# Optimization experiments

Hardware: AMD Instinct MI355X
Metric: run time of the kernel (lower is better)

Reference implementation:

```python
import jax, jax.numpy as jnp
import numpy as np

# Compressed weight shape [O, I] represents a dense [m=2*O, k=2*I] matrix:
#  - 1:2 structured row sparsity: `indices` [O] gives the nonzero dense row ids
#  - 2:4 structured col sparsity: `metadata` [O, I] gives, for each compressed
#    element, its position (0..3) within its group of 4 dense columns
O, I = 4096, 2048          # compressed weight dims (out_features, in_features)
M_DIM, K_DIM = 2 * O, 2 * I  # dense GEMM dims m, k
N_TOK = 4096               # n = input.shape[0]
K_ACT = 2048               # number of active activation rows (multiple of 64)
PAD_MULT = 64


def setup_inputs() -> dict:
    key = jax.random.key(0)
    k1, k2, k3, k4, k5 = jax.random.split(key, 5)
    inp = jax.random.normal(k1, (N_TOK, K_ACT), dtype=jnp.float32)
    # unique, sorted active-feature indices into the dense k dimension
    idx = jnp.sort(jax.random.permutation(k2, K_DIM)[:K_ACT]).astype(jnp.int32)
    # compressed N:M weight values (original uses torch.rand -> uniform [0,1))
    weight = jax.random.uniform(k3, (O, I), dtype=jnp.float32)
    # 1:2 row sparsity: which O of the m dense rows are nonzero
    indices = jnp.sort(jax.random.permutation(k4, M_DIM)[:O]).astype(jnp.int32)
    # 2:4 metadata: per group of 4 dense columns, 2 distinct sorted positions
    G = I // 2
    scores = jax.random.uniform(k5, (O, G, 4))
    metadata = jnp.sort(jnp.argsort(scores, axis=-1)[..., :2], axis=-1)
    metadata = metadata.reshape(O, I).astype(jnp.int32)
    return {"input": inp, "idx": idx, "weight": weight,
            "indices": indices, "metadata": metadata}


def _padding_idx(idx, mult):
    # pad index list to a multiple of `mult` (static shapes)
    pad = (-idx.shape[0]) % mult
    return jnp.pad(idx, (0, pad)), pad


def reference(input, idx, weight, indices, metadata):
    O_, I_ = weight.shape
    m, k, n = 2 * O_, 2 * I_, input.shape[0]
    # ---- decompress N:M weight to dense [m, k] ----
    group_base = (jnp.arange(I_) // 2) * 4                 # [I]
    dense_cols = group_base[None, :] + metadata            # [O, I] in [0, k)
    W = jnp.zeros((m, k), weight.dtype).at[indices[:, None], dense_cols].set(weight)
    # ---- decompress sparse activation to dense B [k, n] ----
    idx_p, pad = _padding_idx(idx, PAD_MULT)
    vals = jnp.pad(input, ((0, 0), (0, pad)))              # [n, K_act+pad]
    B = jnp.zeros((k, n), input.dtype).at[idx_p].add(vals.T)
    # ---- sparse-sparse GEMM (dense-equivalent reference) ----
    return W @ B                                           # [m, n]
```

## Files before the change

kernel.cpp:

```cpp
#include <hip/hip_runtime.h>
#include <hip/hip_bf16.h>
#include <stdint.h>

#define O_DIM   4096
#define I_DIM   2048
#define M_DENSE 8192
#define K_DENSE 4096
#define N_TOK   4096
#define K_ACT   2048

typedef __bf16 bf16x8 __attribute__((ext_vector_type(8)));
typedef float  f32x4  __attribute__((ext_vector_type(4)));

__device__ __forceinline__ unsigned f2bf(float f) {
    unsigned u = __builtin_bit_cast(unsigned, f);
    return (u + 0x7FFFu + ((u >> 16) & 1u)) >> 16;
}

__device__ __forceinline__ void load16(const unsigned short* g, unsigned short* l) {
    __builtin_amdgcn_global_load_lds(
        (__attribute__((address_space(1))) void*)(g),
        (__attribute__((address_space(3))) void*)(l),
        16, 0, 0);
}

__global__ void zero_inactive(const int* __restrict__ indices, float4* __restrict__ out4) {
    int b = blockIdx.x;
    int lo = (b == 0) ? -1 : indices[b - 1];
    int hi = (b == O_DIM) ? M_DENSE : indices[b];
    for (int row = lo + 1; row < hi; ++row) {
        float4* dst = out4 + (size_t)row * (N_TOK / 4);
        for (int c = threadIdx.x; c < N_TOK / 4; c += 256)
            dst[c] = float4{0.f, 0.f, 0.f, 0.f};
    }
}

__global__ __launch_bounds__(256) void prep(const float* __restrict__ weight,
                                            const int* __restrict__ metadata,
                                            const int* __restrict__ idx,
                                            const float* __restrict__ input,
                                            uint4* __restrict__ A2,
                                            uint4* __restrict__ Bbt) {
    if (blockIdx.x >= O_DIM) {
        int gid = (blockIdx.x - O_DIM) * 256 + threadIdx.x;
        const float4* in = (const float4*)input;
        float4 a = in[2 * gid], b = in[2 * gid + 1];
        uint4 u;
        u.x = f2bf(a.x) | (f2bf(a.y) << 16);
        u.y = f2bf(a.z) | (f2bf(a.w) << 16);
        u.z = f2bf(b.x) | (f2bf(b.y) << 16);
        u.w = f2bf(b.z) | (f2bf(b.w) << 16);
        Bbt[gid] = u;
        return;
    }
    __shared__ int   smeta[I_DIM];
    __shared__ float sw[I_DIM];
    int o = blockIdx.x;
    const int4*   mrow = (const int4*)(metadata + (size_t)o * I_DIM);
    const float4* wrow = (const float4*)(weight + (size_t)o * I_DIM);
#pragma unroll
    for (int it = 0; it < I_DIM / 4 / 256; ++it) {
        int i = it * 256 + threadIdx.x;
        *(int4*)(smeta + i * 4) = mrow[i];
        *(float4*)(sw + i * 4)  = wrow[i];
    }
    __syncthreads();
    int j0 = threadIdx.x * 8;
    int4 c0 = *(const int4*)(idx + j0);
    int4 c1 = *(const int4*)(idx + j0 + 4);
    int cs[8] = {c0.x, c0.y, c0.z, c0.w, c1.x, c1.y, c1.z, c1.w};
    unsigned r[8];
#pragma unroll
    for (int u = 0; u < 8; ++u) {
        int c = cs[u];
        int g2 = (c >> 2) * 2;
        int pos = c & 3;
        int m0v = smeta[g2], m1v = smeta[g2 + 1];
        float v = (m0v == pos) ? sw[g2] : ((m1v == pos) ? sw[g2 + 1] : 0.0f);
        r[u] = f2bf(v);
    }
    uint4 packed;
    packed.x = r[0] | (r[1] << 16);
    packed.y = r[2] | (r[3] << 16);
    packed.z = r[4] | (r[5] << 16);
    packed.w = r[6] | (r[7] << 16);
    A2[((size_t)o * K_ACT + j0) >> 3] = packed;
}

__global__ __launch_bounds__(256, 4) void gemm_scatter(
        const unsigned short* __restrict__ A,
        const unsigned short* __restrict__ Bt,
        const int* __restrict__ indices,
        float* __restrict__ out) {
    constexpr int N = N_TOK, K = K_ACT;
    constexpr int TM = 128, TN = 128, BK = 64;
    __shared__ alignas(16) unsigned short sA[TM * BK];
    __shared__ alignas(16) unsigned short sB[TN * BK];

    const int t    = threadIdx.x;
    const int wave = t >> 6;
    const int lane = t & 63;
    const int m0 = blockIdx.y * TM;
    const int n0 = blockIdx.x * TN;

    const int rbase = t >> 3;
    const int sseg  = (t & 7) ^ (rbase & 7);
    const unsigned short* gA = A  + (size_t)(m0 + rbase) * K + sseg * 8;
    const unsigned short* gB = Bt + (size_t)(n0 + rbase) * K + sseg * 8;
    unsigned short* lA = sA + wave * 512;
    unsigned short* lB = sB + wave * 512;

    const int wm   = (wave >> 1) * 64;
    const int wn   = (wave & 1) * 64;
    const int quad = lane >> 4;
    const int lr   = lane & 15;
    const int lr7  = lr & 7;
    const int k0 = (quad ^ lr7) * 8;
    const int k1 = k0 ^ 32;

    f32x4 acc[4][4] = {};

    for (int kk = 0; kk < K; kk += BK) {
        __syncthreads();
#pragma unroll
        for (int q = 0; q < 4; ++q) {
            load16(gA + (size_t)q * (32 * K) + kk, lA + q * 2048);
            load16(gB + (size_t)q * (32 * K) + kk, lB + q * 2048);
        }
        __syncthreads();

        bf16x8 af[4], bf[4];
#pragma unroll
        for (int mi = 0; mi < 4; ++mi)
            af[mi] = *(const bf16x8*)(sA + (wm + mi * 16 + lr) * BK + k0);
#pragma unroll
        for (int ni = 0; ni < 4; ++ni)
            bf[ni] = *(const bf16x8*)(sB + (wn + ni * 16 + lr) * BK + k0);
#pragma unroll
        for (int mi = 0; mi < 4; ++mi)
#pragma unroll
            for (int ni = 0; ni < 4; ++ni)
                acc[mi][ni] = __builtin_amdgcn_mfma_f32_16x16x32_bf16(
                    af[mi], bf[ni], acc[mi][ni], 0, 0, 0);
#pragma unroll
        for (int mi = 0; mi < 4; ++mi)
            af[mi] = *(const bf16x8*)(sA + (wm + mi * 16 + lr) * BK + k1);
#pragma unroll
        for (int ni = 0; ni < 4; ++ni)
            bf[ni] = *(const bf16x8*)(sB + (wn + ni * 16 + lr) * BK + k1);
#pragma unroll
        for (int mi = 0; mi < 4; ++mi)
#pragma unroll
            for (int ni = 0; ni < 4; ++ni)
                acc[mi][ni] = __builtin_amdgcn_mfma_f32_16x16x32_bf16(
                    af[mi], bf[ni], acc[mi][ni], 0, 0, 0);
    }

#pragma unroll
    for (int mi = 0; mi < 4; ++mi) {
#pragma unroll
        for (int r = 0; r < 4; ++r) {
            int gm = m0 + wm + mi * 16 + quad * 4 + r;
            int orow = indices[gm];
            float* op = out + (size_t)orow * N + n0 + wn + lr;
#pragma unroll
            for (int ni = 0; ni < 4; ++ni)
                op[ni * 16] = acc[mi][ni][r];
        }
    }
}

extern "C" void kernel_launch(void* const* d_in, const int* in_sizes, int n_in,
                              void* d_out, int out_size, void* d_ws, size_t ws_size,
                              hipStream_t stream) {
    const float* input    = (const float*)d_in[0];
    const int*   idx      = (const int*)d_in[1];
    const float* weight   = (const float*)d_in[2];
    const int*   indices  = (const int*)d_in[3];
    const int*   metadata = (const int*)d_in[4];
    float* out = (float*)d_out;

    unsigned short* A2  = (unsigned short*)d_ws;
    unsigned short* Bbt = (unsigned short*)((char*)d_ws + (size_t)(16 << 20));

    zero_inactive<<<O_DIM + 1, 256, 0, stream>>>(indices, (float4*)out);
    prep<<<O_DIM + (N_TOK * K_ACT / 8) / 256, 256, 0, stream>>>(
        weight, metadata, idx, input, (uint4*)A2, (uint4*)Bbt);

    dim3 grid(N_TOK / 128, O_DIM / 128);
    gemm_scatter<<<grid, 256, 0, stream>>>(A2, Bbt, indices, out);
}
```

Baseline: 282.5 us.

## Rewrite GEMM as 256x256 tile, 8-wave, 4-stage pipelined kernel; fuse zeroing into prep

```diff
diff --git a/kernel.cpp b/kernel.cpp
--- a/kernel.cpp
+++ b/kernel.cpp
@@ -24,25 +24,29 @@
         16, 0, 0);
 }
 
-__global__ void zero_inactive(const int* __restrict__ indices, float4* __restrict__ out4) {
-    int b = blockIdx.x;
-    int lo = (b == 0) ? -1 : indices[b - 1];
-    int hi = (b == O_DIM) ? M_DENSE : indices[b];
-    for (int row = lo + 1; row < hi; ++row) {
-        float4* dst = out4 + (size_t)row * (N_TOK / 4);
-        for (int c = threadIdx.x; c < N_TOK / 4; c += 256)
-            dst[c] = float4{0.f, 0.f, 0.f, 0.f};
-    }
-}
-
 __global__ __launch_bounds__(256) void prep(const float* __restrict__ weight,
                                             const int* __restrict__ metadata,
                                             const int* __restrict__ idx,
                                             const float* __restrict__ input,
+                                            const int* __restrict__ indices,
                                             uint4* __restrict__ A2,
-                                            uint4* __restrict__ Bbt) {
-    if (blockIdx.x >= O_DIM) {
-        int gid = (blockIdx.x - O_DIM) * 256 + threadIdx.x;
+                                            uint4* __restrict__ Bbt,
+                                            float4* __restrict__ out4) {
+    const int CAST_BLKS = (N_TOK * K_ACT / 8) / 256;
+    int bx = blockIdx.x;
+    if (bx >= O_DIM + CAST_BLKS) {
+        int b = bx - (O_DIM + CAST_BLKS);
+        int lo = (b == 0) ? -1 : indices[b - 1];
+        int hi = (b == O_DIM) ? M_DENSE : indices[b];
+        for (int row = lo + 1; row < hi; ++row) {
+            float4* dst = out4 + (size_t)row * (N_TOK / 4);
+            for (int c = threadIdx.x; c < N_TOK / 4; c += 256)
+                dst[c] = float4{0.f, 0.f, 0.f, 0.f};
+        }
+        return;
+    }
+    if (bx >= O_DIM) {
+        int gid = (bx - O_DIM) * 256 + threadIdx.x;
         const float4* in = (const float4*)input;
         float4 a = in[2 * gid], b = in[2 * gid + 1];
         uint4 u;
@@ -55,7 +59,7 @@
     }
     __shared__ int   smeta[I_DIM];
     __shared__ float sw[I_DIM];
-    int o = blockIdx.x;
+    int o = bx;
     const int4*   mrow = (const int4*)(metadata + (size_t)o * I_DIM);
     const float4* wrow = (const float4*)(weight + (size_t)o * I_DIM);
 #pragma unroll
@@ -87,81 +91,116 @@
     A2[((size_t)o * K_ACT + j0) >> 3] = packed;
 }
 
-__global__ __launch_bounds__(256, 4) void gemm_scatter(
+__global__ __launch_bounds__(512, 2) void gemm8(
         const unsigned short* __restrict__ A,
         const unsigned short* __restrict__ Bt,
         const int* __restrict__ indices,
         float* __restrict__ out) {
     constexpr int N = N_TOK, K = K_ACT;
-    constexpr int TM = 128, TN = 128, BK = 64;
-    __shared__ alignas(16) unsigned short sA[TM * BK];
-    __shared__ alignas(16) unsigned short sB[TN * BK];
-
-    const int t    = threadIdx.x;
-    const int wave = t >> 6;
-    const int lane = t & 63;
-    const int m0 = blockIdx.y * TM;
-    const int n0 = blockIdx.x * TN;
-
-    const int rbase = t >> 3;
-    const int sseg  = (t & 7) ^ (rbase & 7);
-    const unsigned short* gA = A  + (size_t)(m0 + rbase) * K + sseg * 8;
-    const unsigned short* gB = Bt + (size_t)(n0 + rbase) * K + sseg * 8;
-    unsigned short* lA = sA + wave * 512;
-    unsigned short* lB = sB + wave * 512;
-
-    const int wm   = (wave >> 1) * 64;
-    const int wn   = (wave & 1) * 64;
+    constexpr int NT = K / 32;
+    __shared__ alignas(16) unsigned short lds[65536];
+    __shared__ int sidx[256];
+
+    const int tid  = threadIdx.x;
+    const int wave = tid >> 6;
+    const int lane = tid & 63;
     const int quad = lane >> 4;
     const int lr   = lane & 15;
-    const int lr7  = lr & 7;
-    const int k0 = (quad ^ lr7) * 8;
-    const int k1 = k0 ^ 32;
-
-    f32x4 acc[4][4] = {};
-
-    for (int kk = 0; kk < K; kk += BK) {
-        __syncthreads();
-#pragma unroll
-        for (int q = 0; q < 4; ++q) {
-            load16(gA + (size_t)q * (32 * K) + kk, lA + q * 2048);
-            load16(gB + (size_t)q * (32 * K) + kk, lB + q * 2048);
+    const int wm   = (wave >> 2) * 128;
+    const int wn   = (wave & 3) * 64;
+
+    const int bid = blockIdx.x;
+    const int xcd = bid & 7;
+    const int j   = bid >> 3;
+    const int m0  = (j & 15) * 256;
+    const int n0  = (xcd * 2 + (j >> 4)) * 256;
+
+    const int sr_ = tid >> 3;
+    const int cb_ = ((tid & 7) << 4) ^ (((sr_ >> 2) & 1) << 5);
+    const int rh_ = (cb_ >> 6) & 1;
+    const int ke_ = (cb_ & 63) >> 1;
+    const unsigned short* gA0 = A  + (size_t)(m0 + sr_ +      rh_ * 128) * K + ke_;
+    const unsigned short* gA1 = A  + (size_t)(m0 + sr_ + 64 + rh_ * 128) * K + ke_;
+    const unsigned short* gB0 = Bt + (size_t)(n0 + sr_ +      rh_ * 128) * K + ke_;
+    const unsigned short* gB1 = Bt + (size_t)(n0 + sr_ + 64 + rh_ * 128) * K + ke_;
+    unsigned short* dA = lds + wave * 512;
+    unsigned short* dB = lds + 32768 + wave * 512;
+
+    const int laA = wm + lr, srA = laA & 127;
+    const int offA0 = srA * 128 + ((((laA >> 7) << 6) + (quad << 4)) ^ (((srA >> 2) & 1) << 5));
+    const int laB = wn + lr, srB = laB & 127;
+    const int offB0 = srB * 128 + ((((laB >> 7) << 6) + (quad << 4)) ^ (((srB >> 2) & 1) << 5));
+    const char* ldsB = (const char*)lds;
+
+    if (tid < 256) sidx[tid] = indices[m0 + tid];
+
+#pragma unroll
+    for (int pt = 0; pt < 3; ++pt) {
+        load16(gA0 + pt * 32, dA + pt * 8192);
+        load16(gA1 + pt * 32, dA + pt * 8192 + 4096);
+        load16(gB0 + pt * 32, dB + pt * 8192);
+        load16(gB1 + pt * 32, dB + pt * 8192 + 4096);
+    }
+    asm volatile("s_waitcnt vmcnt(8)" ::: "memory");
+    __builtin_amdgcn_s_barrier();
+    asm volatile("" ::: "memory");
+
+    f32x4 acc[8][4] = {};
+
+    for (int tt = 0; tt < NT; tt += 4) {
+#pragma unroll
+        for (int u = 0; u < 4; ++u) {
+            const int t  = tt + u;
+            const int ps = (u + 3) & 3;
+            const int tf = (t + 3 < NT) ? (t + 3) : (t + 3 - NT);
+            bf16x8 af[4], bf[4];
+#pragma unroll
+            for (int mi = 0; mi < 4; ++mi)
+                af[mi] = *(const bf16x8*)(ldsB + u * 16384 + offA0 + mi * 2048);
+#pragma unroll
+            for (int ni = 0; ni < 4; ++ni)
+                bf[ni] = *(const bf16x8*)(ldsB + 65536 + u * 16384 + offB0 + ni * 2048);
+            load16(gA0 + tf * 32, dA + ps * 8192);
+            load16(gA1 + tf * 32, dA + ps * 8192 + 4096);
+            __builtin_amdgcn_s_barrier();
+            asm volatile("s_waitcnt lgkmcnt(0)" ::: "memory");
+            __builtin_amdgcn_s_setprio(1);
+#pragma unroll
+            for (int mi = 0; mi < 4; ++mi)
+#pragma unroll
+                for (int ni = 0; ni < 4; ++ni)
+                    acc[mi][ni] = __builtin_amdgcn_mfma_f32_16x16x32_bf16(
+                        af[mi], bf[ni], acc[mi][ni], 0, 0, 0);
+            __builtin_amdgcn_s_setprio(0);
+            __builtin_amdgcn_s_barrier();
+            asm volatile("" ::: "memory");
+#pragma unroll
+            for (int mi = 0; mi < 4; ++mi)
+                af[mi] = *(const bf16x8*)(ldsB + u * 16384 + offA0 + 8192 + mi * 2048);
+            load16(gB0 + tf * 32, dB + ps * 8192);
+            load16(gB1 + tf * 32, dB + ps * 8192 + 4096);
+            __builtin_amdgcn_s_barrier();
+            asm volatile("s_waitcnt lgkmcnt(0)" ::: "memory");
+            __builtin_amdgcn_s_setprio(1);
+#pragma unroll
+            for (int mi = 0; mi < 4; ++mi)
+#pragma unroll
+                for (int ni = 0; ni < 4; ++ni)
+                    acc[4 + mi][ni] = __builtin_amdgcn_mfma_f32_16x16x32_bf16(
+                        af[mi], bf[ni], acc[4 + mi][ni], 0, 0, 0);
+            __builtin_amdgcn_s_setprio(0);
+            asm volatile("s_waitcnt vmcnt(8)" ::: "memory");
+            __builtin_amdgcn_s_barrier();
+            asm volatile("" ::: "memory");
         }
-        __syncthreads();
-
-        bf16x8 af[4], bf[4];
-#pragma unroll
-        for (int mi = 0; mi < 4; ++mi)
-            af[mi] = *(const bf16x8*)(sA + (wm + mi * 16 + lr) * BK + k0);
-#pragma unroll
-        for (int ni = 0; ni < 4; ++ni)
-            bf[ni] = *(const bf16x8*)(sB + (wn + ni * 16 + lr) * BK + k0);
-#pragma unroll
-        for (int mi = 0; mi < 4; ++mi)
-#pragma unroll
-            for (int ni = 0; ni < 4; ++ni)
-                acc[mi][ni] = __builtin_amdgcn_mfma_f32_16x16x32_bf16(
-                    af[mi], bf[ni], acc[mi][ni], 0, 0, 0);
-#pragma unroll
-        for (int mi = 0; mi < 4; ++mi)
-            af[mi] = *(const bf16x8*)(sA + (wm + mi * 16 + lr) * BK + k1);
-#pragma unroll
-        for (int ni = 0; ni < 4; ++ni)
-            bf[ni] = *(const bf16x8*)(sB + (wn + ni * 16 + lr) * BK + k1);
-#pragma unroll
-        for (int mi = 0; mi < 4; ++mi)
-#pragma unroll
-            for (int ni = 0; ni < 4; ++ni)
-                acc[mi][ni] = __builtin_amdgcn_mfma_f32_16x16x32_bf16(
-                    af[mi], bf[ni], acc[mi][ni], 0, 0, 0);
-    }
-
-#pragma unroll
-    for (int mi = 0; mi < 4; ++mi) {
+    }
+
+#pragma unroll
+    for (int mi = 0; mi < 8; ++mi) {
 #pragma unroll
         for (int r = 0; r < 4; ++r) {
-            int gm = m0 + wm + mi * 16 + quad * 4 + r;
-            int orow = indices[gm];
+            int lm   = wm + mi * 16 + quad * 4 + r;
+            int orow = sidx[lm];
             float* op = out + (size_t)orow * N + n0 + wn + lr;
 #pragma unroll
             for (int ni = 0; ni < 4; ++ni)
@@ -183,10 +222,8 @@
     unsigned short* A2  = (unsigned short*)d_ws;
     unsigned short* Bbt = (unsigned short*)((char*)d_ws + (size_t)(16 << 20));
 
-    zero_inactive<<<O_DIM + 1, 256, 0, stream>>>(indices, (float4*)out);
-    prep<<<O_DIM + (N_TOK * K_ACT / 8) / 256, 256, 0, stream>>>(
-        weight, metadata, idx, input, (uint4*)A2, (uint4*)Bbt);
-
-    dim3 grid(N_TOK / 128, O_DIM / 128);
-    gemm_scatter<<<grid, 256, 0, stream>>>(A2, Bbt, indices, out);
-}
+    prep<<<O_DIM + (N_TOK * K_ACT / 8) / 256 + O_DIM + 1, 256, 0, stream>>>(
+        weight, metadata, idx, input, indices, (uint4*)A2, (uint4*)Bbt, (float4*)out);
+
+    gemm8<<<256, 512, 0, stream>>>(A2, Bbt, indices, out);
+}
```

After: 282.9 us. About the same (+0.2%).
